# Kernel tuning notes

Measured on AMD Instinct MI355X. Metric: run time of the kernel, lower is better.

The kernel has to match this reference:

```python
import jax, jax.numpy as jnp
import numpy as np
from jax import lax

MARGIN = 1.0
LAMDA = 0.003
EPS = 1e-9


def extract_features(f, idx):
    # f: (B,C,h,w); idx: (B,N,2) int with idx[...,0]=x, idx[...,1]=y -> (B*N, C)
    B, N = idx.shape[:2]
    b = jnp.arange(B)[:, None]
    x = idx[..., 0]
    y = idx[..., 1]
    g = f[b, :, y, x]  # (B, N, C)
    return g.reshape(B * N, f.shape[1])


def grad_axis(f, axis):
    # np.gradient along one axis: central differences, one-sided at edges
    fl = jnp.moveaxis(f, axis, 0)
    g = jnp.concatenate([
        fl[1:2] - fl[0:1],
        (fl[2:] - fl[:-2]) * 0.5,
        fl[-1:] - fl[-2:-1],
    ], axis=0)
    return jnp.moveaxis(g, 0, axis)


def contrastive(fa, fb, N, pos):
    diff = fa - fb
    if pos:
        return jnp.sum(diff * diff / N)
    m = jnp.maximum(MARGIN - diff, 0.0)
    return jnp.sum(m * m / N)


def gn_loss(f_t, fb, ub):
    # f_t: (B*N, C) target features; fb: (B,C,h,w); ub: (B,N,2) int matches
    B, N = ub.shape[:2]
    xs = ub  # deterministic stand-in for round(rand + ub) rejection sampling
    f_s = extract_features(fb, xs)
    r = f_s - f_t  # (BN, C)
    fbd = lax.stop_gradient(fb)  # original uses fb.detach() for gradients
    gy = grad_axis(fbd, 2)
    gx = grad_axis(fbd, 3)
    Jx = extract_features(gx, xs)  # (BN, C)
    Jy = extract_features(gy, xs)
    J = jnp.stack([Jx, Jy], axis=-1)  # (BN, C, 2)
    H = jnp.einsum('nci,ncj->nij', J, J) + EPS * jnp.eye(2, dtype=fb.dtype)
    b = jnp.einsum('nci,nc->ni', J, r)  # (BN, 2)
    xsf = xs.reshape(B * N, 2).astype(fb.dtype)
    miu = xsf - jnp.einsum('nij,nj->ni', jnp.linalg.inv(H), b)
    d = ub.reshape(B * N, 2).astype(fb.dtype) - miu
    e1 = 0.5 * jnp.sum(jnp.einsum('na,nab,nb->n', d, H, d))
    log_det = jnp.log(jnp.linalg.det(H))
    e2 = B * N * jnp.log(jnp.asarray(2.0 * np.pi, fb.dtype)) - 0.5 * jnp.sum(log_det)
    return e1 + e2


def gn_forward(F_a, F_b, ka, kb, na, nb):
    N = ka.shape[1]
    fa4 = extract_features(F_a[-1], ka)
    fb4 = extract_features(F_b[-1], kb)
    loss = 0.0
    for i in range(4):
        level = 2 ** (3 - i)
        if i == 3:
            fa_pos, fb_pos = fa4, fb4
        else:
            fa_pos = extract_features(F_a[i], ka // level)
            fb_pos = extract_features(F_b[i], kb // level)
        fa_neg = extract_features(F_a[i], na // level)
        fb_neg = extract_features(F_b[i], nb // level)
        loss_pos = contrastive(fa_pos, fb_pos, N, pos=True)
        loss_neg = contrastive(fa_neg, fb_neg, N, pos=False)
        loss_gn = gn_loss(fa_pos, F_b[i], kb // level)
        loss = loss_pos + loss_neg + LAMDA * loss_gn + loss
    return loss


def setup_inputs() -> dict:
    key = jax.random.key(0)
    ks = jax.random.split(key, 12)
    B, C, H, W, N = 4, 64, 256, 256, 512
    inp = {}
    for j, (name, s) in enumerate([
        ('fa0', 32), ('fa1', 64), ('fa2', 128), ('fa3', 256),
        ('fb0', 32), ('fb1', 64), ('fb2', 128), ('fb3', 256)]):
        inp[name] = jax.random.normal(ks[j], (B, C, s, s), dtype=jnp.float32)
    for j, name in enumerate(['ka', 'kb', 'na', 'nb']):
        inp[name] = jax.random.randint(ks[8 + j], (B, N, 2), 0, 256, dtype=jnp.int32)
    return inp


def reference(fa0, fa1, fa2, fa3, fb0, fb1, fb2, fb3, ka, kb, na, nb):
    F_a = [fa0, fa1, fa2, fa3]
    F_b = [fb0, fb1, fb2, fb3]
    return gn_forward(F_a, F_b, ka, kb, na, nb)
```

## Files before the change

kernel.cpp:

```cpp
#include <hip/hip_runtime.h>

#define MARGIN 1.0f
#define LAMDA  0.003f
#define EPS_H  1e-9f

#define E2_CONST (0.003f * 4.0f * 2048.0f * 1.8378770664093453f)

template <bool NT>
__device__ __forceinline__ float ldf(const float* __restrict__ p) {
    if (NT) return __builtin_nontemporal_load(p);
    return *p;
}

__device__ __forceinline__ float finalize_level(const float* v) {
    const float Hxx = v[2] + EPS_H;
    const float Hxy = v[3];
    const float Hyy = v[4] + EPS_H;
    const float bX  = v[5];
    const float bY  = v[6];
    const float det = Hxx * Hyy - Hxy * Hxy;
    const float e1  = 0.5f * (Hyy * bX * bX - 2.0f * Hxy * bX * bY + Hxx * bY * bY) / det;
    return (v[0] + v[1]) * (1.0f / 512.0f) + LAMDA * (e1 - 0.5f * logf(det));
}

template <bool NT>
__device__ __forceinline__ void gather7(
    const float* __restrict__ fa, const float* __restrict__ fb,
    int2 kA, int2 kB, int2 nA, int2 nB,
    int shift, int S, int plane, float* v)
{
    const int kax = kA.x >> shift, kay = kA.y >> shift;
    const int kbx = kB.x >> shift, kby = kB.y >> shift;
    const int nax = nA.x >> shift, nay = nA.y >> shift;
    const int nbx = nB.x >> shift, nby = nB.y >> shift;

    const int   xm = (kbx > 0)     ? kbx - 1 : 0;
    const int   xp = (kbx < S - 1) ? kbx + 1 : S - 1;
    const float sx = (kbx > 0 && kbx < S - 1) ? 0.5f : 1.0f;
    const int   ym = (kby > 0)     ? kby - 1 : 0;
    const int   yp = (kby < S - 1) ? kby + 1 : S - 1;
    const float sy = (kby > 0 && kby < S - 1) ? 0.5f : 1.0f;

    const float va  = ldf<NT>(fa + plane + kay * S + kax);
    const float vna = ldf<NT>(fa + plane + nay * S + nax);
    const float vb  = ldf<NT>(fb + plane + kby * S + kbx);
    const float vnb = ldf<NT>(fb + plane + nby * S + nbx);
    const float gxm = ldf<NT>(fb + plane + kby * S + xm);
    const float gxp = ldf<NT>(fb + plane + kby * S + xp);
    const float gym = ldf<NT>(fb + plane + ym * S + kbx);
    const float gyp = ldf<NT>(fb + plane + yp * S + kbx);

    const float Jx = (gxp - gxm) * sx;
    const float Jy = (gyp - gym) * sy;

    const float dpos = va - vb;
    const float dneg = vna - vnb;
    const float mneg = fmaxf(MARGIN - dneg, 0.0f);
    const float r    = vb - va;

    v[0] = dpos * dpos;
    v[1] = mneg * mneg;
    v[2] = Jx * Jx;
    v[3] = Jx * Jy;
    v[4] = Jy * Jy;
    v[5] = Jx * r;
    v[6] = Jy * r;
}

__global__ __launch_bounds__(256) void gn_task_kernel(
    const float* __restrict__ fa0, const float* __restrict__ fa1,
    const float* __restrict__ fa2, const float* __restrict__ fa3,
    const float* __restrict__ fb0, const float* __restrict__ fb1,
    const float* __restrict__ fb2, const float* __restrict__ fb3,
    const int* __restrict__ ka, const int* __restrict__ kb,
    const int* __restrict__ na, const int* __restrict__ nb,
    float* __restrict__ out)
{
    __shared__ float wloss[4];

    const int wave  = threadIdx.x >> 6;
    const int lane  = threadIdx.x & 63;
    const int level = wave;
    const int n     = blockIdx.x;
    const int b     = n >> 9;
    const int shift = 3 - level;
    const int S     = 32 << level;

    const int2 kA = ((const int2*)ka)[n];
    const int2 kB = ((const int2*)kb)[n];
    const int2 nA = ((const int2*)na)[n];
    const int2 nB = ((const int2*)nb)[n];

    const int plane = (b * 64 + lane) * (S * S);

    float v[7];
    if (level == 3) {
        gather7<true>(fa3, fb3, kA, kB, nA, nB, 0, 256, plane, v);
    } else if (level == 2) {
        gather7<false>(fa2, fb2, kA, kB, nA, nB, 1, 128, plane, v);
    } else if (level == 1) {
        gather7<false>(fa1, fb1, kA, kB, nA, nB, 2, 64, plane, v);
    } else {
        gather7<false>(fa0, fb0, kA, kB, nA, nB, 3, 32, plane, v);
    }

    #pragma unroll
    for (int mask = 32; mask >= 1; mask >>= 1)
        #pragma unroll
        for (int t = 0; t < 7; ++t)
            v[t] += __shfl_xor(v[t], mask, 64);

    if (lane == 0)
        wloss[wave] = finalize_level(v);

    __syncthreads();
    if (threadIdx.x == 0) {
        float s = wloss[0] + wloss[1] + wloss[2] + wloss[3];
        if (blockIdx.x == 0) s += E2_CONST;
        atomicAdd(out, s);
    }
}

extern "C" void kernel_launch(void* const* d_in, const int* in_sizes, int n_in,
                              void* d_out, int out_size, void* d_ws, size_t ws_size,
                              hipStream_t stream) {
    const float* fa0 = (const float*)d_in[0];
    const float* fa1 = (const float*)d_in[1];
    const float* fa2 = (const float*)d_in[2];
    const float* fa3 = (const float*)d_in[3];
    const float* fb0 = (const float*)d_in[4];
    const float* fb1 = (const float*)d_in[5];
    const float* fb2 = (const float*)d_in[6];
    const float* fb3 = (const float*)d_in[7];
    const int*   ka  = (const int*)d_in[8];
    const int*   kb  = (const int*)d_in[9];
    const int*   na  = (const int*)d_in[10];
    const int*   nb  = (const int*)d_in[11];

    float* out = (float*)d_out;
    hipMemsetAsync(out, 0, sizeof(float), stream);

    gn_task_kernel<<<2048, 256, 0, stream>>>(fa0, fa1, fa2, fa3,
                                             fb0, fb1, fb2, fb3,
                                             ka, kb, na, nb, out);
}
```

Before: 52.61 us.

## Process all four pyramid levels in one wave per keypoint

Each block now has a single 64-lane wave that gathers all four levels, instead of four waves each handling one level. The shared-memory partial sums and the block barrier go away, and each wave issues 32 independent gathers, which raises memory-level parallelism per wave. The level-3 nontemporal load hint is also dropped. In exchange, total wave count falls to a quarter, register pressure rises with 28 accumulators, and the shuffle reduction work per wave grows fourfold.

```diff
diff --git a/kernel.cpp b/kernel.cpp
--- a/kernel.cpp
+++ b/kernel.cpp
@@ -5,12 +5,6 @@
 #define EPS_H  1e-9f
 
 #define E2_CONST (0.003f * 4.0f * 2048.0f * 1.8378770664093453f)
-
-template <bool NT>
-__device__ __forceinline__ float ldf(const float* __restrict__ p) {
-    if (NT) return __builtin_nontemporal_load(p);
-    return *p;
-}
 
 __device__ __forceinline__ float finalize_level(const float* v) {
     const float Hxx = v[2] + EPS_H;
@@ -23,7 +17,6 @@
     return (v[0] + v[1]) * (1.0f / 512.0f) + LAMDA * (e1 - 0.5f * logf(det));
 }
 
-template <bool NT>
 __device__ __forceinline__ void gather7(
     const float* __restrict__ fa, const float* __restrict__ fb,
     int2 kA, int2 kB, int2 nA, int2 nB,
@@ -41,14 +34,14 @@
     const int   yp = (kby < S - 1) ? kby + 1 : S - 1;
     const float sy = (kby > 0 && kby < S - 1) ? 0.5f : 1.0f;
 
-    const float va  = ldf<NT>(fa + plane + kay * S + kax);
-    const float vna = ldf<NT>(fa + plane + nay * S + nax);
-    const float vb  = ldf<NT>(fb + plane + kby * S + kbx);
-    const float vnb = ldf<NT>(fb + plane + nby * S + nbx);
-    const float gxm = ldf<NT>(fb + plane + kby * S + xm);
-    const float gxp = ldf<NT>(fb + plane + kby * S + xp);
-    const float gym = ldf<NT>(fb + plane + ym * S + kbx);
-    const float gyp = ldf<NT>(fb + plane + yp * S + kbx);
+    const float va  = fa[plane + kay * S + kax];
+    const float vna = fa[plane + nay * S + nax];
+    const float vb  = fb[plane + kby * S + kbx];
+    const float vnb = fb[plane + nby * S + nbx];
+    const float gxm = fb[plane + kby * S + xm];
+    const float gxp = fb[plane + kby * S + xp];
+    const float gym = fb[plane + ym * S + kbx];
+    const float gyp = fb[plane + yp * S + kbx];
 
     const float Jx = (gxp - gxm) * sx;
     const float Jy = (gyp - gym) * sy;
@@ -67,7 +60,7 @@
     v[6] = Jy * r;
 }
 
-__global__ __launch_bounds__(256) void gn_task_kernel(
+__global__ __launch_bounds__(64) void gn_task_kernel(
     const float* __restrict__ fa0, const float* __restrict__ fa1,
     const float* __restrict__ fa2, const float* __restrict__ fa3,
     const float* __restrict__ fb0, const float* __restrict__ fb1,
@@ -76,47 +69,37 @@
     const int* __restrict__ na, const int* __restrict__ nb,
     float* __restrict__ out)
 {
-    __shared__ float wloss[4];
-
-    const int wave  = threadIdx.x >> 6;
-    const int lane  = threadIdx.x & 63;
-    const int level = wave;
-    const int n     = blockIdx.x;
-    const int b     = n >> 9;
-    const int shift = 3 - level;
-    const int S     = 32 << level;
+    const int lane = threadIdx.x;
+    const int n    = blockIdx.x;
+    const int b    = n >> 9;
 
     const int2 kA = ((const int2*)ka)[n];
     const int2 kB = ((const int2*)kb)[n];
     const int2 nA = ((const int2*)na)[n];
     const int2 nB = ((const int2*)nb)[n];
 
-    const int plane = (b * 64 + lane) * (S * S);
+    const int base = (b * 64 + lane);
+    const int plane0 = base * (32 * 32);
+    const int plane1 = base * (64 * 64);
+    const int plane2 = base * (128 * 128);
+    const int plane3 = base * (256 * 256);
 
-    float v[7];
-    if (level == 3) {
-        gather7<true>(fa3, fb3, kA, kB, nA, nB, 0, 256, plane, v);
-    } else if (level == 2) {
-        gather7<false>(fa2, fb2, kA, kB, nA, nB, 1, 128, plane, v);
-    } else if (level == 1) {
-        gather7<false>(fa1, fb1, kA, kB, nA, nB, 2, 64, plane, v);
-    } else {
-        gather7<false>(fa0, fb0, kA, kB, nA, nB, 3, 32, plane, v);
-    }
+    float v[28];
+    gather7(fa0, fb0, kA, kB, nA, nB, 3, 32,  plane0, v);
+    gather7(fa1, fb1, kA, kB, nA, nB, 2, 64,  plane1, v + 7);
+    gather7(fa2, fb2, kA, kB, nA, nB, 1, 128, plane2, v + 14);
+    gather7(fa3, fb3, kA, kB, nA, nB, 0, 256, plane3, v + 21);
 
     #pragma unroll
     for (int mask = 32; mask >= 1; mask >>= 1)
         #pragma unroll
-        for (int t = 0; t < 7; ++t)
+        for (int t = 0; t < 28; ++t)
             v[t] += __shfl_xor(v[t], mask, 64);
 
-    if (lane == 0)
-        wloss[wave] = finalize_level(v);
-
-    __syncthreads();
-    if (threadIdx.x == 0) {
-        float s = wloss[0] + wloss[1] + wloss[2] + wloss[3];
-        if (blockIdx.x == 0) s += E2_CONST;
+    if (lane == 0) {
+        float s = finalize_level(v) + finalize_level(v + 7)
+                + finalize_level(v + 14) + finalize_level(v + 21);
+        if (n == 0) s += E2_CONST;
         atomicAdd(out, s);
     }
 }
@@ -140,7 +123,7 @@
     float* out = (float*)d_out;
     hipMemsetAsync(out, 0, sizeof(float), stream);
 
-    gn_task_kernel<<<2048, 256, 0, stream>>>(fa0, fa1, fa2, fa3,
-                                             fb0, fb1, fb2, fb3,
-                                             ka, kb, na, nb, out);
+    gn_task_kernel<<<2048, 64, 0, stream>>>(fa0, fa1, fa2, fa3,
+                                            fb0, fb1, fb2, fb3,
+                                            ka, kb, na, nb, out);
 }
```

Result: slower. 58.97 us (+12.1%).
